# Kernel tuning notes

Measured on AMD Instinct MI355X. Metric: run time of the kernel, lower is better.

Reference implementation:

```python
import jax, jax.numpy as jnp
import numpy as np
from jax import lax

B, T, D = 32, 4096, 256
ZERO_FRAC = 0.3  # fraction of entries zeroed to form missing runs


def setup_inputs() -> dict:
    key = jax.random.key(0)
    k1, k2 = jax.random.split(key)
    vals = jax.random.normal(k1, (B, T, D), dtype=jnp.float32)
    keep = jax.random.uniform(k2, (B, T, D)) > ZERO_FRAC
    x_masked = jnp.where(keep, vals, 0.0)
    return {"x_masked": x_masked}


def reference(x_masked):
    """Linear interpolation over zero runs along time axis, per (b, d).

    Matches torch semantics: for a zero run [start, end), filled with
    torch.linspace(x[start-1], x[end], steps=end-start)  (both endpoints
    included, so filled[start] = x[start-1], filled[end-1] = x[end]).
    Runs touching either sequence boundary are left as zeros.
    """
    x = x_masked
    Bq, Tq, Dq = x.shape
    valid = x != 0  # [B,T,D]
    t = jnp.arange(Tq)[None, :, None]  # [1,T,1]

    # index of last valid entry at or before t (-1 if none)
    prev = lax.cummax(jnp.where(valid, t, -1), axis=1)
    # index of first valid entry at or after t (T if none)
    nxt = lax.cummin(jnp.where(valid, t, Tq), axis=1, reverse=True)

    interior = (~valid) & (prev >= 0) & (nxt < Tq)

    xp = jnp.take_along_axis(x, jnp.clip(prev, 0, Tq - 1), axis=1)  # x[start-1]
    xn = jnp.take_along_axis(x, jnp.clip(nxt, 0, Tq - 1), axis=1)   # x[end]

    run_len = nxt - prev - 1          # L = end - start
    pos = t - prev - 1                # 0-based position within the run
    denom = jnp.maximum(run_len - 1, 1)  # linspace with L points: step = 1/(L-1); L==1 -> xp
    frac = pos.astype(x.dtype) / denom.astype(x.dtype)
    interp = xp + (xn - xp) * frac

    return jnp.where(interior, interp, x)
```

## Files before the change

### kernel.cpp

```cpp
#include <hip/hip_runtime.h>


typedef float f32x4 __attribute__((ext_vector_type(4)));

constexpr int B = 32, T = 4096, D = 256;
constexpr int L = 8;
constexpr int W = 5;
constexpr int NC = T / L;
constexpr int C4 = D / 4;

__global__ __launch_bounds__(256)
void LinearImputer_kernel(const float* __restrict__ x, float* __restrict__ out) {
    const int g  = blockIdx.x * 256 + threadIdx.x;
    const int l  = g & (C4 - 1);
    const int bc = g >> 6;
    const int c  = bc & (NC - 1);
    const int b  = bc >> 9;
    const int t0 = c * L;
    const int t1 = t0 + L;

    const f32x4* __restrict__ x4 = (const f32x4*)x;
    f32x4* __restrict__       o4 = (f32x4*)out;
    const size_t base = ((size_t)b * T) * C4 + l;

    const bool hasB = (c > 0);
    const bool hasF = (c < NC - 1);

    f32x4 hb4[W], hf4[W];
    if (hasB) {
        #pragma unroll
        for (int w = 0; w < W; ++w) hb4[w] = x4[base + (size_t)(t0 - 1 - w) * C4];
    }
    if (hasF) {
        #pragma unroll
        for (int w = 0; w < W; ++w) hf4[w] = x4[base + (size_t)(t1 + w) * C4];
    }
    float v[L][4];
    #pragma unroll
    for (int j = 0; j < L; ++j) {
        f32x4 tv = x4[base + (size_t)(t0 + j) * C4];
        v[j][0] = tv.x; v[j][1] = tv.y; v[j][2] = tv.z; v[j][3] = tv.w;
    }

    int pi[4]; float pv[4];
    #pragma unroll
    for (int cc = 0; cc < 4; ++cc) { pi[cc] = -1; pv[cc] = 0.0f; }
    if (hasB) {
        #pragma unroll
        for (int w = 0; w < W; ++w) {
            float h[4] = {hb4[w].x, hb4[w].y, hb4[w].z, hb4[w].w};
            #pragma unroll
            for (int cc = 0; cc < 4; ++cc)
                if (pi[cc] < 0 && h[cc] != 0.0f) { pi[cc] = t0 - 1 - w; pv[cc] = h[cc]; }
        }
        int pending = 0;
        #pragma unroll
        for (int cc = 0; cc < 4; ++cc)
            if (v[0][cc] == 0.0f && pi[cc] < 0) pending |= (1 << cc);
        if (pending) {
            int tt = t0 - 1 - W;
            while (pending && tt >= 0) {
                f32x4 a0 = x4[base + (size_t)tt * C4];
                const bool has2 = (tt - 1) >= 0;
                f32x4 a1;
                if (has2) a1 = x4[base + (size_t)(tt - 1) * C4];
                float h0[4] = {a0.x, a0.y, a0.z, a0.w};
                #pragma unroll
                for (int cc = 0; cc < 4; ++cc)
                    if (((pending >> cc) & 1) && h0[cc] != 0.0f) {
                        pi[cc] = tt; pv[cc] = h0[cc]; pending &= ~(1 << cc);
                    }
                if (has2 && pending) {
                    float h1[4] = {a1.x, a1.y, a1.z, a1.w};
                    #pragma unroll
                    for (int cc = 0; cc < 4; ++cc)
                        if (((pending >> cc) & 1) && h1[cc] != 0.0f) {
                            pi[cc] = tt - 1; pv[cc] = h1[cc]; pending &= ~(1 << cc);
                        }
                }
                tt -= 2;
            }
        }
    }

    int ni[4]; float nv[4];
    #pragma unroll
    for (int cc = 0; cc < 4; ++cc) { ni[cc] = T; nv[cc] = 0.0f; }
    if (hasF) {
        #pragma unroll
        for (int w = 0; w < W; ++w) {
            float h[4] = {hf4[w].x, hf4[w].y, hf4[w].z, hf4[w].w};
            #pragma unroll
            for (int cc = 0; cc < 4; ++cc)
                if (ni[cc] == T && h[cc] != 0.0f) { ni[cc] = t1 + w; nv[cc] = h[cc]; }
        }
        int pending = 0;
        #pragma unroll
        for (int cc = 0; cc < 4; ++cc)
            if (v[L - 1][cc] == 0.0f && ni[cc] == T) pending |= (1 << cc);
        if (pending) {
            int tt = t1 + W;
            while (pending && tt < T) {
                f32x4 a0 = x4[base + (size_t)tt * C4];
                const bool has2 = (tt + 1) < T;
                f32x4 a1;
                if (has2) a1 = x4[base + (size_t)(tt + 1) * C4];
                float h0[4] = {a0.x, a0.y, a0.z, a0.w};
                #pragma unroll
                for (int cc = 0; cc < 4; ++cc)
                    if (((pending >> cc) & 1) && h0[cc] != 0.0f) {
                        ni[cc] = tt; nv[cc] = h0[cc]; pending &= ~(1 << cc);
                    }
                if (has2 && pending) {
                    float h1[4] = {a1.x, a1.y, a1.z, a1.w};
                    #pragma unroll
                    for (int cc = 0; cc < 4; ++cc)
                        if (((pending >> cc) & 1) && h1[cc] != 0.0f) {
                            ni[cc] = tt + 1; nv[cc] = h1[cc]; pending &= ~(1 << cc);
                        }
                }
                tt += 2;
            }
        }
    }

    #pragma unroll
    for (int j = 0; j < L; ++j) {
        float o[4];
        #pragma unroll
        for (int cc = 0; cc < 4; ++cc) {
            float val = v[j][cc];
            if (val != 0.0f) {
                o[cc] = val; pi[cc] = t0 + j; pv[cc] = val;
            } else {
                int nxi = ni[cc]; float nxv = nv[cc];
                #pragma unroll
                for (int k = L - 1; k > j; --k)
                    if (v[k][cc] != 0.0f) { nxi = t0 + k; nxv = v[k][cc]; }
                if (pi[cc] >= 0 && nxi < T) {
                    int denom = nxi - pi[cc] - 2;
                    if (denom < 1) denom = 1;
                    float frac = __fdividef((float)(t0 + j - pi[cc] - 1), (float)denom);
                    o[cc] = pv[cc] + (nxv - pv[cc]) * frac;
                } else {
                    o[cc] = 0.0f;
                }
            }
        }
        f32x4 ov; ov.x = o[0]; ov.y = o[1]; ov.z = o[2]; ov.w = o[3];
        __builtin_nontemporal_store(ov, &o4[base + (size_t)(t0 + j) * C4]);
    }
}

extern "C" void kernel_launch(void* const* d_in, const int* in_sizes, int n_in,
                              void* d_out, int out_size, void* d_ws, size_t ws_size,
                              hipStream_t stream) {
    const float* x = (const float*)d_in[0];
    float* out = (float*)d_out;
    const int total_threads = B * NC * C4;
    dim3 grid(total_threads / 256), block(256);
    LinearImputer_kernel<<<grid, block, 0, stream>>>(x, out);
}
```

Baseline: 54.14 us.

## Share chunk boundary values across waves via LDS to cut halo reloads

Each 256-thread block now covers four consecutive 8-step time chunks, one per wave. Every wave records the first and last nonzero value per column of its chunk in shared memory, and neighbouring waves look up their previous and next valid values there instead of reloading halo rows from global memory. Only the first and last wave of a block load halos, and the halo depth drops from 5 to 4 rows. The aim is to cut redundant global reads in a kernel that is bound by memory bandwidth. The cost is 16 KB of shared memory per block, a block-wide barrier, and a fallback scan from global memory when no valid value is found in the halo.

Measured after the change: 69.68 us. 28.7% more time.

```diff
diff --git a/kernel.cpp b/kernel.cpp
--- a/kernel.cpp
+++ b/kernel.cpp
@@ -5,35 +5,41 @@
 
 constexpr int B = 32, T = 4096, D = 256;
 constexpr int L = 8;
-constexpr int W = 5;
+constexpr int W = 4;
 constexpr int NC = T / L;
 constexpr int C4 = D / 4;
+constexpr int CPB = 4;
 
 __global__ __launch_bounds__(256)
 void LinearImputer_kernel(const float* __restrict__ x, float* __restrict__ out) {
-    const int g  = blockIdx.x * 256 + threadIdx.x;
-    const int l  = g & (C4 - 1);
-    const int bc = g >> 6;
+    const int tid = threadIdx.x;
+    const int l   = tid & 63;
+    const int wid = tid >> 6;
+    const int bcBase = blockIdx.x * CPB;
+    const int bc = bcBase + wid;
     const int c  = bc & (NC - 1);
     const int b  = bc >> 9;
     const int t0 = c * L;
     const int t1 = t0 + L;
+    const int cFirst  = bcBase & (NC - 1);
+    const int blockT0 = cFirst * L;
+    const int blockT1 = blockT0 + CPB * L;
 
     const f32x4* __restrict__ x4 = (const f32x4*)x;
     f32x4* __restrict__       o4 = (f32x4*)out;
     const size_t base = ((size_t)b * T) * C4 + l;
 
-    const bool hasB = (c > 0);
-    const bool hasF = (c < NC - 1);
-
-    f32x4 hb4[W], hf4[W];
-    if (hasB) {
-        #pragma unroll
-        for (int w = 0; w < W; ++w) hb4[w] = x4[base + (size_t)(t0 - 1 - w) * C4];
-    }
-    if (hasF) {
-        #pragma unroll
-        for (int w = 0; w < W; ++w) hf4[w] = x4[base + (size_t)(t1 + w) * C4];
+    const bool haloB = (wid == 0) && (c > 0);
+    const bool haloF = (wid == CPB - 1) && (c < NC - 1);
+
+    f32x4 hb[W], hf[W];
+    if (haloB) {
+        #pragma unroll
+        for (int w = 0; w < W; ++w) hb[w] = x4[base + (size_t)(t0 - 1 - w) * C4];
+    }
+    if (haloF) {
+        #pragma unroll
+        for (int w = 0; w < W; ++w) hf[w] = x4[base + (size_t)(t1 + w) * C4];
     }
     float v[L][4];
     #pragma unroll
@@ -42,23 +48,64 @@
         v[j][0] = tv.x; v[j][1] = tv.y; v[j][2] = tv.z; v[j][3] = tv.w;
     }
 
+    int topI[4]; float topV[4]; int botI[4]; float botV[4]; int anyZ = 0;
+    #pragma unroll
+    for (int cc = 0; cc < 4; ++cc) { topI[cc] = -1; topV[cc] = 0.0f; botI[cc] = -1; botV[cc] = 0.0f; }
+    #pragma unroll
+    for (int j = 0; j < L; ++j) {
+        #pragma unroll
+        for (int cc = 0; cc < 4; ++cc) {
+            float val = v[j][cc];
+            if (val != 0.0f) {
+                if (topI[cc] < 0) { topI[cc] = t0 + j; topV[cc] = val; }
+                botI[cc] = t0 + j; botV[cc] = val;
+            } else {
+                anyZ |= (1 << cc);
+            }
+        }
+    }
+
+    __shared__ int   sTI[CPB][D]; __shared__ float sTV[CPB][D];
+    __shared__ int   sBI[CPB][D]; __shared__ float sBV[CPB][D];
+    #pragma unroll
+    for (int cc = 0; cc < 4; ++cc) {
+        const int col = l * 4 + cc;
+        sTI[wid][col] = topI[cc]; sTV[wid][col] = topV[cc];
+        sBI[wid][col] = botI[cc]; sBV[wid][col] = botV[cc];
+    }
+    __syncthreads();
+
     int pi[4]; float pv[4];
     #pragma unroll
     for (int cc = 0; cc < 4; ++cc) { pi[cc] = -1; pv[cc] = 0.0f; }
-    if (hasB) {
+    #pragma unroll
+    for (int k = 1; k < CPB; ++k) {
+        if (wid >= k) {
+            const int kw = wid - k;
+            #pragma unroll
+            for (int cc = 0; cc < 4; ++cc)
+                if (pi[cc] < 0) {
+                    int bi = sBI[kw][l * 4 + cc];
+                    if (bi >= 0) { pi[cc] = bi; pv[cc] = sBV[kw][l * 4 + cc]; }
+                }
+        }
+    }
+    if (haloB) {
         #pragma unroll
         for (int w = 0; w < W; ++w) {
-            float h[4] = {hb4[w].x, hb4[w].y, hb4[w].z, hb4[w].w};
+            float h[4] = {hb[w].x, hb[w].y, hb[w].z, hb[w].w};
             #pragma unroll
             for (int cc = 0; cc < 4; ++cc)
                 if (pi[cc] < 0 && h[cc] != 0.0f) { pi[cc] = t0 - 1 - w; pv[cc] = h[cc]; }
         }
+    }
+    {
         int pending = 0;
         #pragma unroll
         for (int cc = 0; cc < 4; ++cc)
-            if (v[0][cc] == 0.0f && pi[cc] < 0) pending |= (1 << cc);
-        if (pending) {
-            int tt = t0 - 1 - W;
+            if (((anyZ >> cc) & 1) && pi[cc] < 0) pending |= (1 << cc);
+        if (pending && cFirst > 0) {
+            int tt = haloB ? (t0 - 1 - W) : (blockT0 - 1);
             while (pending && tt >= 0) {
                 f32x4 a0 = x4[base + (size_t)tt * C4];
                 const bool has2 = (tt - 1) >= 0;
@@ -86,20 +133,34 @@
     int ni[4]; float nv[4];
     #pragma unroll
     for (int cc = 0; cc < 4; ++cc) { ni[cc] = T; nv[cc] = 0.0f; }
-    if (hasF) {
+    #pragma unroll
+    for (int k = 1; k < CPB; ++k) {
+        if (wid + k < CPB) {
+            const int kw = wid + k;
+            #pragma unroll
+            for (int cc = 0; cc < 4; ++cc)
+                if (ni[cc] == T) {
+                    int ti = sTI[kw][l * 4 + cc];
+                    if (ti >= 0) { ni[cc] = ti; nv[cc] = sTV[kw][l * 4 + cc]; }
+                }
+        }
+    }
+    if (haloF) {
         #pragma unroll
         for (int w = 0; w < W; ++w) {
-            float h[4] = {hf4[w].x, hf4[w].y, hf4[w].z, hf4[w].w};
+            float h[4] = {hf[w].x, hf[w].y, hf[w].z, hf[w].w};
             #pragma unroll
             for (int cc = 0; cc < 4; ++cc)
                 if (ni[cc] == T && h[cc] != 0.0f) { ni[cc] = t1 + w; nv[cc] = h[cc]; }
         }
+    }
+    {
         int pending = 0;
         #pragma unroll
         for (int cc = 0; cc < 4; ++cc)
-            if (v[L - 1][cc] == 0.0f && ni[cc] == T) pending |= (1 << cc);
-        if (pending) {
-            int tt = t1 + W;
+            if (((anyZ >> cc) & 1) && ni[cc] == T) pending |= (1 << cc);
+        if (pending && blockT1 < T) {
+            int tt = haloF ? (t1 + W) : blockT1;
             while (pending && tt < T) {
                 f32x4 a0 = x4[base + (size_t)tt * C4];
                 const bool has2 = (tt + 1) < T;
@@ -157,7 +218,7 @@
                               hipStream_t stream) {
     const float* x = (const float*)d_in[0];
     float* out = (float*)d_out;
-    const int total_threads = B * NC * C4;
-    dim3 grid(total_threads / 256), block(256);
+    const int total_blocks = (B * NC) / CPB;
+    dim3 grid(total_blocks), block(256);
     LinearImputer_kernel<<<grid, block, 0, stream>>>(x, out);
 }
```
